# Kernel tuning notes

Measured on AMD Instinct MI355X. Metric: run time of the kernel, lower is better.

The kernel has to match this reference:

```python
import jax, jax.numpy as jnp
import numpy as np

N = 4096       # voc_size
D = 256        # emb_dim
NEG = -9e15    # pyGAT mask value
ALPHA = 0.2    # LeakyReLU slope


def _row_normalize(a):
    rs = a.sum(axis=1, keepdims=True)
    inv = jnp.where(rs > 0, 1.0 / rs, 0.0)
    return a * inv


def setup_inputs() -> dict:
    key = jax.random.key(0)
    ks = jax.random.split(key, 10)
    # sparse-ish symmetric adjacency, then self-loops + row-normalize (GraphAT.normalize)
    raw = (jax.random.uniform(ks[0], (N, N)) < 0.01).astype(jnp.float32)
    raw = jnp.maximum(raw, raw.T)
    adj = _row_normalize(raw + jnp.eye(N, dtype=jnp.float32))
    x = jax.random.normal(ks[1], (N, N), dtype=jnp.float32) * 0.05
    def w(k, i, o):
        return jax.random.normal(k, (i, o), dtype=jnp.float32) * (1.0 / np.sqrt(i))
    return {
        "x": x, "adj": adj,
        "W11": w(ks[2], N, D), "a11": jax.random.normal(ks[3], (2 * D, 1), jnp.float32) * 0.1,
        "W12": w(ks[4], D, D), "a12": jax.random.normal(ks[5], (2 * D, 1), jnp.float32) * 0.1,
        "W21": w(ks[6], D, D), "a21": jax.random.normal(ks[7], (2 * D, 1), jnp.float32) * 0.1,
        "W22": w(ks[8], D, D), "a22": jax.random.normal(ks[9], (2 * D, 1), jnp.float32) * 0.1,
    }


def _gat_layer(h, adj, W, a):
    # Wh: [N, d_out]
    Wh = h @ W
    d_out = W.shape[1]
    f_src = Wh @ a[:d_out]          # [N, 1]
    f_dst = Wh @ a[d_out:]          # [N, 1]
    e = jax.nn.leaky_relu(f_src + f_dst.T, ALPHA)   # [N, N]
    e = jnp.where(adj > 0, e, NEG)
    attn = jax.nn.softmax(e, axis=1)
    return attn @ Wh                # [N, d_out]


def _gat(h, adj, Wa, aa, Wb, ab):
    # pyGAT GAT: multi-head (1 head) + ELU, then output attention layer + ELU
    h = jax.nn.elu(_gat_layer(h, adj, Wa, aa))
    return jax.nn.elu(_gat_layer(h, adj, Wb, ab))


def reference(x, adj, W11, a11, W12, a12, W21, a21, W22, a22):
    h = _gat(x, adj, W11, a11, W12, a12)
    h = jax.nn.relu(h)              # dropout(p=0.3) is identity in eval mode
    return _gat(h, adj, W21, a21, W22, a22)
```

## Files before the change

### kernel.cpp

```cpp
#include <hip/hip_runtime.h>
#include <hip/hip_bf16.h>
#include <cstdint>
#include <cstddef>

#define NV 4096
#define DE 256
#define MAXNNZ 192

typedef __attribute__((ext_vector_type(8))) short bf16x8;
typedef __attribute__((ext_vector_type(4))) float f32x4;

__device__ __forceinline__ unsigned short f2bf(float f) {
    unsigned int u = __float_as_uint(f);
    u += 0x7fff + ((u >> 16) & 1);
    return (unsigned short)(u >> 16);
}
__device__ __forceinline__ float bf2f(unsigned short h) {
    return __uint_as_float(((unsigned int)h) << 16);
}

__global__ __launch_bounds__(256) void build_csr(const float* __restrict__ adj,
                                                 int* __restrict__ cols,
                                                 int* __restrict__ nnz)
{
    int wave = threadIdx.x >> 6;
    int lane = threadIdx.x & 63;
    int row  = blockIdx.x * 4 + wave;
    const float* arow = adj + (size_t)row * NV;
    int* crow = cols + (size_t)row * MAXNNZ;
    int base = 0;
    for (int c0 = 0; c0 < NV; c0 += 64) {
        float v = arow[c0 + lane];
        bool pred = v > 0.0f;
        unsigned long long m = __ballot(pred);
        int idx = base + __popcll(m & ((1ull << lane) - 1ull));
        if (pred && idx < MAXNNZ) crow[idx] = c0 + lane;
        base += __popcll(m);
    }
    if (lane == 0) nnz[row] = base < MAXNNZ ? base : MAXNNZ;
}

__global__ __launch_bounds__(256) void transp_split(const float* __restrict__ W,
                                                    unsigned short* __restrict__ bh,
                                                    unsigned short* __restrict__ bl,
                                                    int K)
{
    __shared__ float tile[32][33];
    const int k0 = blockIdx.x * 32, n0 = blockIdx.y * 32;
    const int t = threadIdx.x;
    {
        int r = t >> 3, cq = t & 7;
        float4 v = *(const float4*)&W[(size_t)(k0 + r) * DE + n0 + cq * 4];
        tile[r][cq * 4 + 0] = v.x;
        tile[r][cq * 4 + 1] = v.y;
        tile[r][cq * 4 + 2] = v.z;
        tile[r][cq * 4 + 3] = v.w;
    }
    __syncthreads();
    {
        int nl = t >> 3, kq = t & 7;
        ushort4 hv, lv;
        float x0 = tile[kq * 4 + 0][nl];
        float x1 = tile[kq * 4 + 1][nl];
        float x2 = tile[kq * 4 + 2][nl];
        float x3 = tile[kq * 4 + 3][nl];
        hv.x = f2bf(x0); lv.x = f2bf(x0 - bf2f(hv.x));
        hv.y = f2bf(x1); lv.y = f2bf(x1 - bf2f(hv.y));
        hv.z = f2bf(x2); lv.z = f2bf(x2 - bf2f(hv.z));
        hv.w = f2bf(x3); lv.w = f2bf(x3 - bf2f(hv.w));
        size_t o = (size_t)(n0 + nl) * K + k0 + kq * 4;
        *(ushort4*)&bh[o] = hv;
        *(ushort4*)&bl[o] = lv;
    }
}

#define BM 64
#define BN 128
#define BK 32

__global__ __launch_bounds__(256) void gemm_split(const float* __restrict__ A,
                                                  const unsigned short* __restrict__ Bh,
                                                  const unsigned short* __restrict__ Bl,
                                                  float* __restrict__ C,
                                                  int K, int Kchunk)
{
    __shared__ __align__(16) unsigned short sA[64 * 64];
    __shared__ __align__(16) unsigned short sB[128 * 64];

    const int t    = threadIdx.x;
    const int lane = t & 63;
    const int wid  = t >> 6;
    const int wr   = wid >> 1;
    const int wc   = wid & 1;
    const int bn   = blockIdx.x * BN;
    const int bm   = blockIdx.y * BM;
    const int kz   = blockIdx.z;
    const int kbeg = kz * Kchunk;
    const int nsteps = Kchunk / BK;

    const int ar = t >> 2;
    const int as = t & 3;
    const int br = t >> 1;
    const int bhf = t & 1;

    const float*          Ap  = A  + (size_t)(bm + ar) * K + kbeg + as * 8;
    const unsigned short* Bhp = Bh + (size_t)(bn + br) * K + kbeg + bhf * 16;
    const unsigned short* Blp = Bl + (size_t)(bn + br) * K + kbeg + bhf * 16;

    const int aw_h = ar * 64 + (((as)     ^ (ar & 7)) << 3);
    const int aw_l = ar * 64 + (((as | 4) ^ (ar & 7)) << 3);
    const int bs0  = bhf * 2;
    const int bw_h0 = br * 64 + (((bs0)         ^ (br & 7)) << 3);
    const int bw_h1 = br * 64 + (((bs0 + 1)     ^ (br & 7)) << 3);
    const int bw_l0 = br * 64 + ((((bs0) | 4)   ^ (br & 7)) << 3);
    const int bw_l1 = br * 64 + ((((bs0 + 1) | 4) ^ (br & 7)) << 3);

    const int fr = lane & 15, fsub = lane >> 4;
    const int arow0 = wr * 32 + fr;
    const int arow1 = arow0 + 16;
    const int ard0h = arow0 * 64 + (((fsub)     ^ (arow0 & 7)) << 3);
    const int ard0l = arow0 * 64 + (((fsub | 4) ^ (arow0 & 7)) << 3);
    const int ard1h = arow1 * 64 + (((fsub)     ^ (arow1 & 7)) << 3);
    const int ard1l = arow1 * 64 + (((fsub | 4) ^ (arow1 & 7)) << 3);

    float4 a0 = *(const float4*)(Ap);
    float4 a1 = *(const float4*)(Ap + 4);
    bf16x8 g_bh0 = *(const bf16x8*)(Bhp);
    bf16x8 g_bh1 = *(const bf16x8*)(Bhp + 8);
    bf16x8 g_bl0 = *(const bf16x8*)(Blp);
    bf16x8 g_bl1 = *(const bf16x8*)(Blp + 8);

    f32x4 acc[2][4];
#pragma unroll
    for (int i = 0; i < 2; ++i)
#pragma unroll
        for (int j = 0; j < 4; ++j) acc[i][j] = (f32x4){0.f, 0.f, 0.f, 0.f};

    for (int s = 0; s < nsteps; ++s) {
        __syncthreads();
        {
            float xs0 = a0.x, xs1 = a0.y, xs2 = a0.z, xs3 = a0.w;
            float xs4 = a1.x, xs5 = a1.y, xs6 = a1.z, xs7 = a1.w;
            bf16x8 hv, lv;
            unsigned short h;
            h = f2bf(xs0); hv[0] = (short)h; lv[0] = (short)f2bf(xs0 - bf2f(h));
            h = f2bf(xs1); hv[1] = (short)h; lv[1] = (short)f2bf(xs1 - bf2f(h));
            h = f2bf(xs2); hv[2] = (short)h; lv[2] = (short)f2bf(xs2 - bf2f(h));
            h = f2bf(xs3); hv[3] = (short)h; lv[3] = (short)f2bf(xs3 - bf2f(h));
            h = f2bf(xs4); hv[4] = (short)h; lv[4] = (short)f2bf(xs4 - bf2f(h));
            h = f2bf(xs5); hv[5] = (short)h; lv[5] = (short)f2bf(xs5 - bf2f(h));
            h = f2bf(xs6); hv[6] = (short)h; lv[6] = (short)f2bf(xs6 - bf2f(h));
            h = f2bf(xs7); hv[7] = (short)h; lv[7] = (short)f2bf(xs7 - bf2f(h));
            *(bf16x8*)&sA[aw_h] = hv;
            *(bf16x8*)&sA[aw_l] = lv;
        }
        *(bf16x8*)&sB[bw_h0] = g_bh0;
        *(bf16x8*)&sB[bw_h1] = g_bh1;
        *(bf16x8*)&sB[bw_l0] = g_bl0;
        *(bf16x8*)&sB[bw_l1] = g_bl1;
        __syncthreads();

        if (s + 1 < nsteps) {
            Ap += BK; Bhp += BK; Blp += BK;
            a0 = *(const float4*)(Ap);
            a1 = *(const float4*)(Ap + 4);
            g_bh0 = *(const bf16x8*)(Bhp);
            g_bh1 = *(const bf16x8*)(Bhp + 8);
            g_bl0 = *(const bf16x8*)(Blp);
            g_bl1 = *(const bf16x8*)(Blp + 8);
        }

        bf16x8 ah0 = *(const bf16x8*)&sA[ard0h];
        bf16x8 al0 = *(const bf16x8*)&sA[ard0l];
        bf16x8 ah1 = *(const bf16x8*)&sA[ard1h];
        bf16x8 al1 = *(const bf16x8*)&sA[ard1l];
        bf16x8 bhv[4], blv[4];
#pragma unroll
        for (int ni = 0; ni < 4; ++ni) {
            int n = wc * 64 + ni * 16 + fr;
            bhv[ni] = *(const bf16x8*)&sB[n * 64 + (((fsub)     ^ (n & 7)) << 3)];
            blv[ni] = *(const bf16x8*)&sB[n * 64 + (((fsub | 4) ^ (n & 7)) << 3)];
        }
#pragma unroll
        for (int ni = 0; ni < 4; ++ni) {
            acc[0][ni] = __builtin_amdgcn_mfma_f32_16x16x32_bf16(ah0, bhv[ni], acc[0][ni], 0, 0, 0);
            acc[0][ni] = __builtin_amdgcn_mfma_f32_16x16x32_bf16(ah0, blv[ni], acc[0][ni], 0, 0, 0);
            acc[0][ni] = __builtin_amdgcn_mfma_f32_16x16x32_bf16(al0, bhv[ni], acc[0][ni], 0, 0, 0);
            acc[1][ni] = __builtin_amdgcn_mfma_f32_16x16x32_bf16(ah1, bhv[ni], acc[1][ni], 0, 0, 0);
            acc[1][ni] = __builtin_amdgcn_mfma_f32_16x16x32_bf16(ah1, blv[ni], acc[1][ni], 0, 0, 0);
            acc[1][ni] = __builtin_amdgcn_mfma_f32_16x16x32_bf16(al1, bhv[ni], acc[1][ni], 0, 0, 0);
        }
    }

    float* Cb = C + (size_t)kz * NV * DE;
#pragma unroll
    for (int mi = 0; mi < 2; ++mi) {
#pragma unroll
        for (int ni = 0; ni < 4; ++ni) {
            int row = bm + wr * 32 + mi * 16 + (fsub << 2);
            int col = bn + wc * 64 + ni * 16 + fr;
#pragma unroll
            for (int i = 0; i < 4; ++i)
                Cb[(size_t)(row + i) * DE + col] = acc[mi][ni][i];
        }
    }
}

__global__ __launch_bounds__(256) void reduce_fsd(const float* __restrict__ Cp,
                                                  const float* __restrict__ a,
                                                  float* __restrict__ Wh,
                                                  float* __restrict__ fs,
                                                  float* __restrict__ fd)
{
    int wid = threadIdx.x >> 6, lane = threadIdx.x & 63;
    int row = blockIdx.x * 4 + wid;
    size_t idx = (size_t)row * DE + lane * 4;
    float4 p0 = *(const float4*)&Cp[idx];
    float4 p1 = *(const float4*)&Cp[(size_t)NV * DE + idx];
    float4 w;
    w.x = p0.x + p1.x; w.y = p0.y + p1.y; w.z = p0.z + p1.z; w.w = p0.w + p1.w;
    *(float4*)&Wh[idx] = w;
    float4 at = *(const float4*)&a[lane * 4];
    float4 ab = *(const float4*)&a[DE + lane * 4];
    float s = w.x * at.x + w.y * at.y + w.z * at.z + w.w * at.w;
    float d = w.x * ab.x + w.y * ab.y + w.z * ab.z + w.w * ab.w;
#pragma unroll
    for (int off = 32; off; off >>= 1) {
        s += __shfl_down(s, off);
        d += __shfl_down(d, off);
    }
    if (lane == 0) { fs[row] = s; fd[row] = d; }
}

__global__ __launch_bounds__(256) void fsd_kernel(const float* __restrict__ Wh,
                                                  const float* __restrict__ a,
                                                  float* __restrict__ fs,
                                                  float* __restrict__ fd)
{
    int wave = threadIdx.x >> 6;
    int lane = threadIdx.x & 63;
    int row  = blockIdx.x * 4 + wave;
    float4 w  = *(const float4*)&Wh[(size_t)row * DE + lane * 4];
    float4 at = *(const float4*)&a[lane * 4];
    float4 ab = *(const float4*)&a[DE + lane * 4];
    float s = w.x * at.x + w.y * at.y + w.z * at.z + w.w * at.w;
    float d = w.x * ab.x + w.y * ab.y + w.z * ab.z + w.w * ab.w;
#pragma unroll
    for (int off = 32; off; off >>= 1) {
        s += __shfl_down(s, off);
        d += __shfl_down(d, off);
    }
    if (lane == 0) { fs[row] = s; fd[row] = d; }
}

template <int ACT>
__global__ __launch_bounds__(256) void attn_spmm(const float* __restrict__ Wh,
                                                 const float* __restrict__ fs,
                                                 const float* __restrict__ fd,
                                                 const int* __restrict__ cols,
                                                 const int* __restrict__ nnzArr,
                                                 float* __restrict__ out)
{
    __shared__ float p[MAXNNZ];
    __shared__ int   ci[MAXNNZ];
    __shared__ float red[4];

    const int row = blockIdx.x;
    const int t   = threadIdx.x;
    const int lane = t & 63;
    const int wv   = t >> 6;
    const int n   = nnzArr[row];
    const int* rc = cols + (size_t)row * MAXNNZ;
    const float fsi = fs[row];

    float lm = -1e30f;
    for (int j = t; j < n; j += 256) {
        int c = rc[j];
        ci[j] = c;
        float e = fsi + fd[c];
        e = (e >= 0.0f) ? e : 0.2f * e;
        p[j] = e;
        lm = fmaxf(lm, e);
    }
#pragma unroll
    for (int off = 32; off; off >>= 1) lm = fmaxf(lm, __shfl_down(lm, off));
    if (lane == 0) red[wv] = lm;
    __syncthreads();
    const float m = fmaxf(fmaxf(red[0], red[1]), fmaxf(red[2], red[3]));
    __syncthreads();

    float ls = 0.0f;
    for (int j = t; j < n; j += 256) {
        float pe = expf(p[j] - m);
        p[j] = pe;
        ls += pe;
    }
#pragma unroll
    for (int off = 32; off; off >>= 1) ls += __shfl_down(ls, off);
    if (lane == 0) red[wv] = ls;
    __syncthreads();
    const float invZ = 1.0f / (red[0] + red[1] + red[2] + red[3]);

    const int d = t;
    float acc = 0.0f;
    int j = 0;
    for (; j + 4 <= n; j += 4) {
        float p0 = p[j], p1 = p[j + 1], p2 = p[j + 2], p3 = p[j + 3];
        int   c0 = ci[j], c1 = ci[j + 1], c2 = ci[j + 2], c3 = ci[j + 3];
        acc = fmaf(p0, Wh[(size_t)c0 * DE + d], acc);
        acc = fmaf(p1, Wh[(size_t)c1 * DE + d], acc);
        acc = fmaf(p2, Wh[(size_t)c2 * DE + d], acc);
        acc = fmaf(p3, Wh[(size_t)c3 * DE + d], acc);
    }
    for (; j < n; ++j) acc = fmaf(p[j], Wh[(size_t)ci[j] * DE + d], acc);
    acc *= invZ;

    float r;
    if (ACT == 0) r = (acc > 0.0f) ? acc : expm1f(acc);
    else          r = (acc > 0.0f) ? acc : 0.0f;
    out[(size_t)row * DE + d] = r;
}

extern "C" void kernel_launch(void* const* d_in, const int* in_sizes, int n_in,
                              void* d_out, int out_size, void* d_ws, size_t ws_size,
                              hipStream_t stream)
{
    const float* x   = (const float*)d_in[0];
    const float* adj = (const float*)d_in[1];
    const float* W11 = (const float*)d_in[2];
    const float* a11 = (const float*)d_in[3];
    const float* W12 = (const float*)d_in[4];
    const float* a12 = (const float*)d_in[5];
    const float* W21 = (const float*)d_in[6];
    const float* a21 = (const float*)d_in[7];
    const float* W22 = (const float*)d_in[8];
    const float* a22 = (const float*)d_in[9];
    float* out = (float*)d_out;

    char* ws = (char*)d_ws;
    size_t off = 0;
    int*   cols = (int*)(ws + off);            off += (size_t)NV * MAXNNZ * 4;
    int*   nnz  = (int*)(ws + off);            off += 16 * 1024;
    float* fs   = (float*)(ws + off);          off += 16 * 1024;
    float* fd   = (float*)(ws + off);          off += 16 * 1024;
    float* Wh   = (float*)(ws + off);          off += (size_t)NV * DE * 4;
    float* hA   = (float*)(ws + off);          off += (size_t)NV * DE * 4;
    unsigned short* BtH = (unsigned short*)(ws + off); off += (size_t)DE * NV * 2;
    unsigned short* BtL = (unsigned short*)(ws + off); off += (size_t)DE * NV * 2;
    float* Cpart = (float*)(ws + off);

    build_csr<<<NV / 4, 256, 0, stream>>>(adj, cols, nnz);

    transp_split<<<dim3(NV / 32, DE / 32), 256, 0, stream>>>(W11, BtH, BtL, NV);
    gemm_split<<<dim3(DE / BN, NV / BM, 2), 256, 0, stream>>>(x, BtH, BtL, Cpart, NV, NV / 2);
    reduce_fsd<<<NV / 4, 256, 0, stream>>>(Cpart, a11, Wh, fs, fd);
    attn_spmm<0><<<NV, 256, 0, stream>>>(Wh, fs, fd, cols, nnz, hA);

    transp_split<<<dim3(DE / 32, DE / 32), 256, 0, stream>>>(W12, BtH, BtL, DE);
    gemm_split<<<dim3(DE / BN, NV / BM, 1), 256, 0, stream>>>(hA, BtH, BtL, Wh, DE, DE);
    fsd_kernel<<<NV / 4, 256, 0, stream>>>(Wh, a12, fs, fd);
    attn_spmm<1><<<NV, 256, 0, stream>>>(Wh, fs, fd, cols, nnz, hA);

    transp_split<<<dim3(DE / 32, DE / 32), 256, 0, stream>>>(W21, BtH, BtL, DE);
    gemm_split<<<dim3(DE / BN, NV / BM, 1), 256, 0, stream>>>(hA, BtH, BtL, Wh, DE, DE);
    fsd_kernel<<<NV / 4, 256, 0, stream>>>(Wh, a21, fs, fd);
    attn_spmm<0><<<NV, 256, 0, stream>>>(Wh, fs, fd, cols, nnz, hA);

    transp_split<<<dim3(DE / 32, DE / 32), 256, 0, stream>>>(W22, BtH, BtL, DE);
    gemm_split<<<dim3(DE / BN, NV / BM, 1), 256, 0, stream>>>(hA, BtH, BtL, Wh, DE, DE);
    fsd_kernel<<<NV / 4, 256, 0, stream>>>(Wh, a22, fs, fd);
    attn_spmm<0><<<NV, 256, 0, stream>>>(Wh, fs, fd, cols, nnz, out);
}
```

Before: 228.3 us.

## Shrink GEMM tile, raise split-K, and vectorize attention SpMM across waves

The GEMM tile width drops from 128 to 64 columns and split-K rises to 4 for the big first layer and 2 for the small layers. This puts more blocks on the GPU, which has many CUs. The reduce kernel now takes a variable split count and replaces the separate fsd kernel. The attention SpMM gives each wave a strided subset of neighbors, loads float4 rows, and combines the per-wave partial sums through shared memory. This adds memory-level parallelism to the gather. The cost is extra partial-sum traffic, and each GEMM tile reuses less data.

```diff
diff --git a/kernel.cpp b/kernel.cpp
--- a/kernel.cpp
+++ b/kernel.cpp
@@ -75,7 +75,7 @@
 }
 
 #define BM 64
-#define BN 128
+#define BN 64
 #define BK 32
 
 __global__ __launch_bounds__(256) void gemm_split(const float* __restrict__ A,
@@ -85,7 +85,7 @@
                                                   int K, int Kchunk)
 {
     __shared__ __align__(16) unsigned short sA[64 * 64];
-    __shared__ __align__(16) unsigned short sB[128 * 64];
+    __shared__ __align__(16) unsigned short sB[64 * 64];
 
     const int t    = threadIdx.x;
     const int lane = t & 63;
@@ -100,20 +100,17 @@
 
     const int ar = t >> 2;
     const int as = t & 3;
-    const int br = t >> 1;
-    const int bhf = t & 1;
+    const int br = t >> 2;
+    const int bq = t & 3;
 
     const float*          Ap  = A  + (size_t)(bm + ar) * K + kbeg + as * 8;
-    const unsigned short* Bhp = Bh + (size_t)(bn + br) * K + kbeg + bhf * 16;
-    const unsigned short* Blp = Bl + (size_t)(bn + br) * K + kbeg + bhf * 16;
-
-    const int aw_h = ar * 64 + (((as)     ^ (ar & 7)) << 3);
-    const int aw_l = ar * 64 + (((as | 4) ^ (ar & 7)) << 3);
-    const int bs0  = bhf * 2;
-    const int bw_h0 = br * 64 + (((bs0)         ^ (br & 7)) << 3);
-    const int bw_h1 = br * 64 + (((bs0 + 1)     ^ (br & 7)) << 3);
-    const int bw_l0 = br * 64 + ((((bs0) | 4)   ^ (br & 7)) << 3);
-    const int bw_l1 = br * 64 + ((((bs0 + 1) | 4) ^ (br & 7)) << 3);
+    const unsigned short* Bhp = Bh + (size_t)(bn + br) * K + kbeg + bq * 8;
+    const unsigned short* Blp = Bl + (size_t)(bn + br) * K + kbeg + bq * 8;
+
+    const int aw_h = ar * 64 + (((as)      ^ (ar & 7)) << 3);
+    const int aw_l = ar * 64 + (((as | 4)  ^ (ar & 7)) << 3);
+    const int bw_h = br * 64 + (((bq)      ^ (br & 7)) << 3);
+    const int bw_l = br * 64 + (((bq | 4)  ^ (br & 7)) << 3);
 
     const int fr = lane & 15, fsub = lane >> 4;
     const int arow0 = wr * 32 + fr;
@@ -122,19 +119,23 @@
     const int ard0l = arow0 * 64 + (((fsub | 4) ^ (arow0 & 7)) << 3);
     const int ard1h = arow1 * 64 + (((fsub)     ^ (arow1 & 7)) << 3);
     const int ard1l = arow1 * 64 + (((fsub | 4) ^ (arow1 & 7)) << 3);
+    const int brow0 = wc * 32 + fr;
+    const int brow1 = brow0 + 16;
+    const int brd0h = brow0 * 64 + (((fsub)     ^ (brow0 & 7)) << 3);
+    const int brd0l = brow0 * 64 + (((fsub | 4) ^ (brow0 & 7)) << 3);
+    const int brd1h = brow1 * 64 + (((fsub)     ^ (brow1 & 7)) << 3);
+    const int brd1l = brow1 * 64 + (((fsub | 4) ^ (brow1 & 7)) << 3);
 
     float4 a0 = *(const float4*)(Ap);
     float4 a1 = *(const float4*)(Ap + 4);
-    bf16x8 g_bh0 = *(const bf16x8*)(Bhp);
-    bf16x8 g_bh1 = *(const bf16x8*)(Bhp + 8);
-    bf16x8 g_bl0 = *(const bf16x8*)(Blp);
-    bf16x8 g_bl1 = *(const bf16x8*)(Blp + 8);
-
-    f32x4 acc[2][4];
+    bf16x8 g_bh = *(const bf16x8*)(Bhp);
+    bf16x8 g_bl = *(const bf16x8*)(Blp);
+
+    f32x4 acc[2][2];
 #pragma unroll
     for (int i = 0; i < 2; ++i)
 #pragma unroll
-        for (int j = 0; j < 4; ++j) acc[i][j] = (f32x4){0.f, 0.f, 0.f, 0.f};
+        for (int j = 0; j < 2; ++j) acc[i][j] = (f32x4){0.f, 0.f, 0.f, 0.f};
 
     for (int s = 0; s < nsteps; ++s) {
         __syncthreads();
@@ -154,51 +155,48 @@
             *(bf16x8*)&sA[aw_h] = hv;
             *(bf16x8*)&sA[aw_l] = lv;
         }
-        *(bf16x8*)&sB[bw_h0] = g_bh0;
-        *(bf16x8*)&sB[bw_h1] = g_bh1;
-        *(bf16x8*)&sB[bw_l0] = g_bl0;
-        *(bf16x8*)&sB[bw_l1] = g_bl1;
+        *(bf16x8*)&sB[bw_h] = g_bh;
+        *(bf16x8*)&sB[bw_l] = g_bl;
         __syncthreads();
 
         if (s + 1 < nsteps) {
             Ap += BK; Bhp += BK; Blp += BK;
             a0 = *(const float4*)(Ap);
             a1 = *(const float4*)(Ap + 4);
-            g_bh0 = *(const bf16x8*)(Bhp);
-            g_bh1 = *(const bf16x8*)(Bhp + 8);
-            g_bl0 = *(const bf16x8*)(Blp);
-            g_bl1 = *(const bf16x8*)(Blp + 8);
+            g_bh = *(const bf16x8*)(Bhp);
+            g_bl = *(const bf16x8*)(Blp);
         }
 
         bf16x8 ah0 = *(const bf16x8*)&sA[ard0h];
         bf16x8 al0 = *(const bf16x8*)&sA[ard0l];
         bf16x8 ah1 = *(const bf16x8*)&sA[ard1h];
         bf16x8 al1 = *(const bf16x8*)&sA[ard1l];
-        bf16x8 bhv[4], blv[4];
-#pragma unroll
-        for (int ni = 0; ni < 4; ++ni) {
-            int n = wc * 64 + ni * 16 + fr;
-            bhv[ni] = *(const bf16x8*)&sB[n * 64 + (((fsub)     ^ (n & 7)) << 3)];
-            blv[ni] = *(const bf16x8*)&sB[n * 64 + (((fsub | 4) ^ (n & 7)) << 3)];
-        }
-#pragma unroll
-        for (int ni = 0; ni < 4; ++ni) {
-            acc[0][ni] = __builtin_amdgcn_mfma_f32_16x16x32_bf16(ah0, bhv[ni], acc[0][ni], 0, 0, 0);
-            acc[0][ni] = __builtin_amdgcn_mfma_f32_16x16x32_bf16(ah0, blv[ni], acc[0][ni], 0, 0, 0);
-            acc[0][ni] = __builtin_amdgcn_mfma_f32_16x16x32_bf16(al0, bhv[ni], acc[0][ni], 0, 0, 0);
-            acc[1][ni] = __builtin_amdgcn_mfma_f32_16x16x32_bf16(ah1, bhv[ni], acc[1][ni], 0, 0, 0);
-            acc[1][ni] = __builtin_amdgcn_mfma_f32_16x16x32_bf16(ah1, blv[ni], acc[1][ni], 0, 0, 0);
-            acc[1][ni] = __builtin_amdgcn_mfma_f32_16x16x32_bf16(al1, bhv[ni], acc[1][ni], 0, 0, 0);
-        }
+        bf16x8 bh0 = *(const bf16x8*)&sB[brd0h];
+        bf16x8 bl0 = *(const bf16x8*)&sB[brd0l];
+        bf16x8 bh1 = *(const bf16x8*)&sB[brd1h];
+        bf16x8 bl1 = *(const bf16x8*)&sB[brd1l];
+
+        acc[0][0] = __builtin_amdgcn_mfma_f32_16x16x32_bf16(ah0, bh0, acc[0][0], 0, 0, 0);
+        acc[0][0] = __builtin_amdgcn_mfma_f32_16x16x32_bf16(ah0, bl0, acc[0][0], 0, 0, 0);
+        acc[0][0] = __builtin_amdgcn_mfma_f32_16x16x32_bf16(al0, bh0, acc[0][0], 0, 0, 0);
+        acc[0][1] = __builtin_amdgcn_mfma_f32_16x16x32_bf16(ah0, bh1, acc[0][1], 0, 0, 0);
+        acc[0][1] = __builtin_amdgcn_mfma_f32_16x16x32_bf16(ah0, bl1, acc[0][1], 0, 0, 0);
+        acc[0][1] = __builtin_amdgcn_mfma_f32_16x16x32_bf16(al0, bh1, acc[0][1], 0, 0, 0);
+        acc[1][0] = __builtin_amdgcn_mfma_f32_16x16x32_bf16(ah1, bh0, acc[1][0], 0, 0, 0);
+        acc[1][0] = __builtin_amdgcn_mfma_f32_16x16x32_bf16(ah1, bl0, acc[1][0], 0, 0, 0);
+        acc[1][0] = __builtin_amdgcn_mfma_f32_16x16x32_bf16(al1, bh0, acc[1][0], 0, 0, 0);
+        acc[1][1] = __builtin_amdgcn_mfma_f32_16x16x32_bf16(ah1, bh1, acc[1][1], 0, 0, 0);
+        acc[1][1] = __builtin_amdgcn_mfma_f32_16x16x32_bf16(ah1, bl1, acc[1][1], 0, 0, 0);
+        acc[1][1] = __builtin_amdgcn_mfma_f32_16x16x32_bf16(al1, bh1, acc[1][1], 0, 0, 0);
     }
 
     float* Cb = C + (size_t)kz * NV * DE;
 #pragma unroll
     for (int mi = 0; mi < 2; ++mi) {
 #pragma unroll
-        for (int ni = 0; ni < 4; ++ni) {
+        for (int ni = 0; ni < 2; ++ni) {
             int row = bm + wr * 32 + mi * 16 + (fsub << 2);
-            int col = bn + wc * 64 + ni * 16 + fr;
+            int col = bn + wc * 32 + ni * 16 + fr;
 #pragma unroll
             for (int i = 0; i < 4; ++i)
                 Cb[(size_t)(row + i) * DE + col] = acc[mi][ni][i];
@@ -210,37 +208,18 @@
                                                   const float* __restrict__ a,
                                                   float* __restrict__ Wh,
                                                   float* __restrict__ fs,
-                                                  float* __restrict__ fd)
+                                                  float* __restrict__ fd,
+                                                  int S)
 {
     int wid = threadIdx.x >> 6, lane = threadIdx.x & 63;
     int row = blockIdx.x * 4 + wid;
     size_t idx = (size_t)row * DE + lane * 4;
-    float4 p0 = *(const float4*)&Cp[idx];
-    float4 p1 = *(const float4*)&Cp[(size_t)NV * DE + idx];
-    float4 w;
-    w.x = p0.x + p1.x; w.y = p0.y + p1.y; w.z = p0.z + p1.z; w.w = p0.w + p1.w;
+    float4 w = *(const float4*)&Cp[idx];
+    for (int s = 1; s < S; ++s) {
+        float4 p = *(const float4*)&Cp[(size_t)s * NV * DE + idx];
+        w.x += p.x; w.y += p.y; w.z += p.z; w.w += p.w;
+    }
     *(float4*)&Wh[idx] = w;
-    float4 at = *(const float4*)&a[lane * 4];
-    float4 ab = *(const float4*)&a[DE + lane * 4];
-    float s = w.x * at.x + w.y * at.y + w.z * at.z + w.w * at.w;
-    float d = w.x * ab.x + w.y * ab.y + w.z * ab.z + w.w * ab.w;
-#pragma unroll
-    for (int off = 32; off; off >>= 1) {
-        s += __shfl_down(s, off);
-        d += __shfl_down(d, off);
-    }
-    if (lane == 0) { fs[row] = s; fd[row] = d; }
-}
-
-__global__ __launch_bounds__(256) void fsd_kernel(const float* __restrict__ Wh,
-                                                  const float* __restrict__ a,
-                                                  float* __restrict__ fs,
-                                                  float* __restrict__ fd)
-{
-    int wave = threadIdx.x >> 6;
-    int lane = threadIdx.x & 63;
-    int row  = blockIdx.x * 4 + wave;
-    float4 w  = *(const float4*)&Wh[(size_t)row * DE + lane * 4];
     float4 at = *(const float4*)&a[lane * 4];
     float4 ab = *(const float4*)&a[DE + lane * 4];
     float s = w.x * at.x + w.y * at.y + w.z * at.z + w.w * at.w;
@@ -264,6 +243,7 @@
     __shared__ float p[MAXNNZ];
     __shared__ int   ci[MAXNNZ];
     __shared__ float red[4];
+    __shared__ float part[4][DE];
 
     const int row = blockIdx.x;
     const int t   = threadIdx.x;
@@ -301,24 +281,40 @@
     __syncthreads();
     const float invZ = 1.0f / (red[0] + red[1] + red[2] + red[3]);
 
-    const int d = t;
-    float acc = 0.0f;
-    int j = 0;
-    for (; j + 4 <= n; j += 4) {
-        float p0 = p[j], p1 = p[j + 1], p2 = p[j + 2], p3 = p[j + 3];
-        int   c0 = ci[j], c1 = ci[j + 1], c2 = ci[j + 2], c3 = ci[j + 3];
-        acc = fmaf(p0, Wh[(size_t)c0 * DE + d], acc);
-        acc = fmaf(p1, Wh[(size_t)c1 * DE + d], acc);
-        acc = fmaf(p2, Wh[(size_t)c2 * DE + d], acc);
-        acc = fmaf(p3, Wh[(size_t)c3 * DE + d], acc);
-    }
-    for (; j < n; ++j) acc = fmaf(p[j], Wh[(size_t)ci[j] * DE + d], acc);
-    acc *= invZ;
-
+    const int d4 = lane * 4;
+    f32x4 acc = (f32x4){0.f, 0.f, 0.f, 0.f};
+    int j = wv;
+    for (; j + 4 < n; j += 8) {
+        float pj0 = p[j];     int c0 = ci[j];
+        float pj1 = p[j + 4]; int c1 = ci[j + 4];
+        float4 w0 = *(const float4*)&Wh[(size_t)c0 * DE + d4];
+        float4 w1 = *(const float4*)&Wh[(size_t)c1 * DE + d4];
+        acc.x = fmaf(pj0, w0.x, acc.x);
+        acc.y = fmaf(pj0, w0.y, acc.y);
+        acc.z = fmaf(pj0, w0.z, acc.z);
+        acc.w = fmaf(pj0, w0.w, acc.w);
+        acc.x = fmaf(pj1, w1.x, acc.x);
+        acc.y = fmaf(pj1, w1.y, acc.y);
+        acc.z = fmaf(pj1, w1.z, acc.z);
+        acc.w = fmaf(pj1, w1.w, acc.w);
+    }
+    for (; j < n; j += 4) {
+        float pj = p[j]; int c = ci[j];
+        float4 w0 = *(const float4*)&Wh[(size_t)c * DE + d4];
+        acc.x = fmaf(pj, w0.x, acc.x);
+        acc.y = fmaf(pj, w0.y, acc.y);
+        acc.z = fmaf(pj, w0.z, acc.z);
+        acc.w = fmaf(pj, w0.w, acc.w);
+    }
+    *(f32x4*)&part[wv][d4] = acc;
+    __syncthreads();
+
+    float v = (part[0][t] + part[1][t]) + (part[2][t] + part[3][t]);
+    v *= invZ;
     float r;
-    if (ACT == 0) r = (acc > 0.0f) ? acc : expm1f(acc);
-    else          r = (acc > 0.0f) ? acc : 0.0f;
-    out[(size_t)row * DE + d] = r;
+    if (ACT == 0) r = (v > 0.0f) ? v : expm1f(v);
+    else          r = (v > 0.0f) ? v : 0.0f;
+    out[(size_t)row * DE + t] = r;
 }
 
 extern "C" void kernel_launch(void* const* d_in, const int* in_sizes, int n_in,
@@ -352,22 +348,22 @@
     build_csr<<<NV / 4, 256, 0, stream>>>(adj, cols, nnz);
 
     transp_split<<<dim3(NV / 32, DE / 32), 256, 0, stream>>>(W11, BtH, BtL, NV);
-    gemm_split<<<dim3(DE / BN, NV / BM, 2), 256, 0, stream>>>(x, BtH, BtL, Cpart, NV, NV / 2);
-    reduce_fsd<<<NV / 4, 256, 0, stream>>>(Cpart, a11, Wh, fs, fd);
+    gemm_split<<<dim3(DE / BN, NV / BM, 4), 256, 0, stream>>>(x, BtH, BtL, Cpart, NV, NV / 4);
+    reduce_fsd<<<NV / 4, 256, 0, stream>>>(Cpart, a11, Wh, fs, fd, 4);
     attn_spmm<0><<<NV, 256, 0, stream>>>(Wh, fs, fd, cols, nnz, hA);
 
     transp_split<<<dim3(DE / 32, DE / 32), 256, 0, stream>>>(W12, BtH, BtL, DE);
-    gemm_split<<<dim3(DE / BN, NV / BM, 1), 256, 0, stream>>>(hA, BtH, BtL, Wh, DE, DE);
-    fsd_kernel<<<NV / 4, 256, 0, stream>>>(Wh, a12, fs, fd);
+    gemm_split<<<dim3(DE / BN, NV / BM, 2), 256, 0, stream>>>(hA, BtH, BtL, Cpart, DE, DE / 2);
+    reduce_fsd<<<NV / 4, 256, 0, stream>>>(Cpart, a12, Wh, fs, fd, 2);
     attn_spmm<1><<<NV, 256, 0, stream>>>(Wh, fs, fd, cols, nnz, hA);
 
     transp_split<<<dim3(DE / 32, DE / 32), 256, 0, stream>>>(W21, BtH, BtL, DE);
-    gemm_split<<<dim3(DE / BN, NV / BM, 1), 256, 0, stream>>>(hA, BtH, BtL, Wh, DE, DE);
-    fsd_kernel<<<NV / 4, 256, 0, stream>>>(Wh, a21, fs, fd);
+    gemm_split<<<dim3(DE / BN, NV / BM, 2), 256, 0, stream>>>(hA, BtH, BtL, Cpart, DE, DE / 2);
+    reduce_fsd<<<NV / 4, 256, 0, stream>>>(Cpart, a21, Wh, fs, fd, 2);
     attn_spmm<0><<<NV, 256, 0, stream>>>(Wh, fs, fd, cols, nnz, hA);
 
     transp_split<<<dim3(DE / 32, DE / 32), 256, 0, stream>>>(W22, BtH, BtL, DE);
-    gemm_split<<<dim3(DE / BN, NV / BM, 1), 256, 0, stream>>>(hA, BtH, BtL, Wh, DE, DE);
-    fsd_kernel<<<NV / 4, 256, 0, stream>>>(Wh, a22, fs, fd);
+    gemm_split<<<dim3(DE / BN, NV / BM, 2), 256, 0, stream>>>(hA, BtH, BtL, Cpart, DE, DE / 2);
+    reduce_fsd<<<NV / 4, 256, 0, stream>>>(Cpart, a22, Wh, fs, fd, 2);
     attn_spmm<0><<<NV, 256, 0, stream>>>(Wh, fs, fd, cols, nnz, out);
 }
```

After: 194.1 us. 1.18x faster.
